# Kernel tuning notes

Hardware: AMD Instinct MI355X
Metric: run time of the kernel (lower is better)

## Reference

```python
import jax, jax.numpy as jnp
import numpy as np

BN_EPS = 1e-3      # Keras BatchNormalization default epsilon
LRELU_ALPHA = 0.3  # Keras LeakyReLU default alpha


def _bn(x, gamma, beta, mean, var):
    # inference-mode batch norm over the feature (last) axis
    return gamma * (x - mean) * jax.lax.rsqrt(var + BN_EPS) + beta


def _gcn(x, adj, w, b):
    # spektral GCNConv: A_hat @ (X @ W) + b   (adj assumed pre-normalized)
    xw = jnp.einsum('bnf,fc->bnc', x, w)
    return jnp.einsum('bnm,bmc->bnc', adj, xw) + b


def _lrelu(x):
    return jnp.where(x >= 0, x, LRELU_ALPHA * x)


def setup_inputs() -> dict:
    key = jax.random.key(0)
    ks = jax.random.split(key, 12)
    B, N, C = 16, 1024, 256
    x = jax.random.normal(ks[0], (B, N, C), dtype=jnp.float32)
    # roughly row-normalized dense adjacency (stands in for D^-1/2 (A+I) D^-1/2)
    adj = jax.random.uniform(ks[1], (B, N, N), dtype=jnp.float32) / N
    s = 1.0 / np.sqrt(C)
    return {
        'x': x,
        'adj': adj,
        'bn1_gamma': jnp.ones((C,), jnp.float32),
        'bn1_beta': jnp.zeros((C,), jnp.float32),
        'bn1_mean': jax.random.normal(ks[2], (C,), jnp.float32) * 0.1,
        'bn1_var': jax.random.uniform(ks[3], (C,), jnp.float32) + 0.5,
        'w1': jax.random.normal(ks[4], (C, C), jnp.float32) * s,
        'b1': jnp.zeros((C,), jnp.float32),
        'bn2_gamma': jnp.ones((C,), jnp.float32),
        'bn2_beta': jnp.zeros((C,), jnp.float32),
        'bn2_mean': jax.random.normal(ks[5], (C,), jnp.float32) * 0.1,
        'bn2_var': jax.random.uniform(ks[6], (C,), jnp.float32) + 0.5,
        'w2': jax.random.normal(ks[7], (C, C), jnp.float32) * s,
        'b2': jnp.zeros((C,), jnp.float32),
        'w_skip': jax.random.normal(ks[8], (C, C), jnp.float32) * s,
        'b_skip': jnp.zeros((C,), jnp.float32),
    }


def reference(x, adj, bn1_gamma, bn1_beta, bn1_mean, bn1_var, w1, b1,
              bn2_gamma, bn2_beta, bn2_mean, bn2_var, w2, b2, w_skip, b_skip):
    h = _bn(x, bn1_gamma, bn1_beta, bn1_mean, bn1_var)          # BN(input)
    out = _lrelu(_gcn(h, adj, w1, b1))                          # GCNConv + LeakyReLU
    out = _bn(out, bn2_gamma, bn2_beta, bn2_mean, bn2_var)      # BN
    out = _lrelu(_gcn(out, adj, w2, b2))                        # GCNConv + LeakyReLU
    skip = _gcn(h, adj, w_skip, b_skip)                         # skip GCNConv on BN(input)
    # Dropout is identity at inference
    return out + skip
```

## Files before the change

### kernel.cpp

```cpp
#include <hip/hip_runtime.h>

#define LRELU_ALPHA 0.3f
#define BN_EPS 1e-3f

using u16 = unsigned short;
using u32 = unsigned int;

typedef __attribute__((ext_vector_type(8))) short bf16x8;
typedef __attribute__((ext_vector_type(4))) float f32x4;

struct alignas(8) U16x4 { u16 x, y, z, w; };

__device__ __forceinline__ u16 f2bf(float f) {
  union { float f; u32 u; } v; v.f = f;
  u32 b = v.u;
  b += 0x7FFFu + ((b >> 16) & 1u);
  return (u16)(b >> 16);
}
__device__ __forceinline__ float bf2f(u16 h) {
  union { u32 u; float f; } v; v.u = ((u32)h) << 16;
  return v.f;
}

typedef const __attribute__((address_space(1))) void* gas_ptr;
typedef __attribute__((address_space(3))) void* las_ptr;

__device__ __forceinline__ void gload16(const void* g, void* l) {
  __builtin_amdgcn_global_load_lds((gas_ptr)g, (las_ptr)l, 16, 0, 0);
}

template <int K>
__device__ __forceinline__ void gemm_core(const u16* __restrict__ A,
                                          const u16* __restrict__ B,
                                          u16* lds, f32x4 (&acc)[4][4]) {
  const int t = threadIdx.x, lane = t & 63, wid = t >> 6;
  const int wm = (wid >> 1) * 64, wn = (wid & 1) * 64;
  const int lrow = lane & 15, lk = (lane >> 4) * 8;
  const int r0 = t >> 3, ce = (t & 7) * 8, lo = wid * 512;
  u16* ldsA = lds;
  u16* ldsB = lds + 8192;
#pragma unroll 1
  for (int kt = 0; kt < K / 64; ++kt) {
    const u16* gA = A + kt * 64;
    const u16* gB = B + kt * 64;
#pragma unroll
    for (int cc = 0; cc < 4; ++cc) {
      gload16(gA + (size_t)(cc * 32 + r0) * K + ce, ldsA + cc * 2048 + lo);
      gload16(gB + (size_t)(cc * 32 + r0) * K + ce, ldsB + cc * 2048 + lo);
    }
    asm volatile("s_waitcnt vmcnt(0)" ::: "memory");
    __syncthreads();
#pragma unroll
    for (int kk = 0; kk < 2; ++kk) {
      bf16x8 a[4], b[4];
#pragma unroll
      for (int i = 0; i < 4; ++i)
        a[i] = *(const bf16x8*)(ldsA + (wm + i * 16 + lrow) * 64 + kk * 32 + lk);
#pragma unroll
      for (int i = 0; i < 4; ++i)
        b[i] = *(const bf16x8*)(ldsB + (wn + i * 16 + lrow) * 64 + kk * 32 + lk);
#pragma unroll
      for (int i = 0; i < 4; ++i)
#pragma unroll
        for (int j = 0; j < 4; ++j)
          acc[i][j] = __builtin_amdgcn_mfma_f32_16x16x32_bf16(a[i], b[j], acc[i][j], 0, 0, 0);
    }
    __syncthreads();
  }
}

template <int K>
__device__ __forceinline__ void gemm_core64(const u16* __restrict__ A,
                                            const u16* __restrict__ B,
                                            u16* lds, f32x4 (&acc)[2][4]) {
  const int t = threadIdx.x, lane = t & 63, wid = t >> 6;
  const int wm = wid * 32;
  const int lrow = lane & 15, lk = (lane >> 4) * 8;
  const int r0 = t >> 3, ce = (t & 7) * 8, lo = wid * 512;
  u16* ldsA = lds;
  u16* ldsB = lds + 8192;
#pragma unroll 1
  for (int kt = 0; kt < K / 64; ++kt) {
    const u16* gA = A + kt * 64;
    const u16* gB = B + kt * 64;
#pragma unroll
    for (int cc = 0; cc < 4; ++cc)
      gload16(gA + (size_t)(cc * 32 + r0) * K + ce, ldsA + cc * 2048 + lo);
#pragma unroll
    for (int cc = 0; cc < 2; ++cc)
      gload16(gB + (size_t)(cc * 32 + r0) * K + ce, ldsB + cc * 2048 + lo);
    asm volatile("s_waitcnt vmcnt(0)" ::: "memory");
    __syncthreads();
#pragma unroll
    for (int kk = 0; kk < 2; ++kk) {
      bf16x8 a[2], b[4];
#pragma unroll
      for (int i = 0; i < 2; ++i)
        a[i] = *(const bf16x8*)(ldsA + (wm + i * 16 + lrow) * 64 + kk * 32 + lk);
#pragma unroll
      for (int j = 0; j < 4; ++j)
        b[j] = *(const bf16x8*)(ldsB + (j * 16 + lrow) * 64 + kk * 32 + lk);
#pragma unroll
      for (int i = 0; i < 2; ++i)
#pragma unroll
        for (int j = 0; j < 4; ++j)
          acc[i][j] = __builtin_amdgcn_mfma_f32_16x16x32_bf16(a[i], b[j], acc[i][j], 0, 0, 0);
    }
    __syncthreads();
  }
}

#define ACC_INIT(R)                                 \
  f32x4 acc[R][4];                                  \
  _Pragma("unroll") for (int i_ = 0; i_ < R; ++i_)  \
  _Pragma("unroll") for (int j_ = 0; j_ < 4; ++j_)  \
      acc[i_][j_] = {0.f, 0.f, 0.f, 0.f};

__global__ __launch_bounds__(256) void k_prep_h(
    const float* __restrict__ w1, const float* __restrict__ wsk, const float* __restrict__ w2,
    const float* __restrict__ g1, const float* __restrict__ be1,
    const float* __restrict__ m1, const float* __restrict__ v1,
    const float* __restrict__ g2, const float* __restrict__ be2,
    const float* __restrict__ m2, const float* __restrict__ v2,
    const float* __restrict__ x,
    u16* __restrict__ wcatT, u16* __restrict__ w2T,
    float* __restrict__ s2, float* __restrict__ t2c, u16* __restrict__ h_bf) {
  int bid = blockIdx.x;
  if (bid < 768) {
    if (bid == 0) {
      int c = threadIdx.x;
      float a2 = g2[c] * rsqrtf(v2[c] + BN_EPS);
      s2[c] = a2;
      t2c[c] = be2[c] - m2[c] * a2;
    }
    int i = bid * 256 + threadIdx.x;
    if (i < 131072) {
      int co = i >> 8, ci = i & 255;
      const float* w = (co < 256) ? w1 : wsk;
      wcatT[i] = f2bf(w[ci * 256 + (co & 255)]);
    } else {
      int k = i - 131072;
      int co = k >> 8, ci = k & 255;
      w2T[k] = f2bf(w2[ci * 256 + co]);
    }
  } else {
    int base = (bid - 768) * 256 + threadIdx.x;
    int c0 = (base << 2) & 255;
    float sc[4], sh[4];
#pragma unroll
    for (int u = 0; u < 4; ++u) {
      int c = c0 + u;
      float a = g1[c] * rsqrtf(v1[c] + BN_EPS);
      sc[u] = a;
      sh[u] = be1[c] - m1[c] * a;
    }
#pragma unroll
    for (int j = 0; j < 16; ++j) {
      int k = j * 65536 + base;
      float4 v = ((const float4*)x)[k];
      U16x4 o = {f2bf(v.x * sc[0] + sh[0]), f2bf(v.y * sc[1] + sh[1]),
                 f2bf(v.z * sc[2] + sh[2]), f2bf(v.w * sc[3] + sh[3])};
      ((U16x4*)h_bf)[k] = o;
    }
  }
}

__global__ __launch_bounds__(256) void k_xw_cvt(const float* __restrict__ adj,
                                                u16* __restrict__ adj_bf,
                                                const u16* __restrict__ h_bf,
                                                const u16* __restrict__ wcatT,
                                                u16* __restrict__ hwT) {
  __shared__ u16 lds[17408];
  const int bid = blockIdx.x;
  const int r = bid % 5;
  if (r == 4) {
    const int stripe = bid / 5;
    const float4* src = (const float4*)adj + (size_t)stripe * 32768;
    U16x4* dst = (U16x4*)adj_bf + (size_t)stripe * 32768;
    for (int i = threadIdx.x; i < 32768; i += 256) {
      float4 v = src[i];
      U16x4 o = {f2bf(v.x), f2bf(v.y), f2bf(v.z), f2bf(v.w)};
      dst[i] = o;
    }
    return;
  }
  const int mt = bid / 5, nt = r;
  ACC_INIT(4);
  gemm_core<256>(h_bf + (size_t)mt * 128 * 256, wcatT + (size_t)nt * 128 * 256, lds, acc);

  const int t = threadIdx.x, lane = t & 63, wid = t >> 6;
  const int row0 = (wid >> 1) * 64 + (lane >> 4) * 4;
  const int col0 = (wid & 1) * 64 + (lane & 15);
  __syncthreads();
  u16* tl = lds;
#pragma unroll
  for (int j = 0; j < 4; ++j) {
    int co_l = col0 + j * 16;
#pragma unroll
    for (int i = 0; i < 4; ++i)
#pragma unroll
      for (int q = 0; q < 4; ++q)
        tl[co_l * 136 + row0 + i * 16 + q] = f2bf(acc[i][j][q]);
  }
  __syncthreads();
  const int rw = t >> 4, seg = t & 15;
  const int b = mt >> 3, nb = (mt & 7) * 128;
#pragma unroll
  for (int p = 0; p < 8; ++p) {
    int co_l = p * 16 + rw;
    *(bf16x8*)(hwT + (((size_t)(b * 512 + nt * 128 + co_l)) << 10) + nb + seg * 8) =
        *(const bf16x8*)(tl + co_l * 136 + seg * 8);
  }
}

__global__ __launch_bounds__(256) void k_big1(const u16* __restrict__ adj_bf,
                                              const u16* __restrict__ hwT,
                                              const float* __restrict__ b1,
                                              const float* __restrict__ bsk,
                                              const float* __restrict__ s2,
                                              const float* __restrict__ t2c,
                                              u16* __restrict__ u2b,
                                              u16* __restrict__ skipb) {
  __shared__ u16 lds[17408];
  ACC_INIT(4);
  const int mt = blockIdx.x, nt = blockIdx.y, bz = blockIdx.z;
  gemm_core<1024>(adj_bf + ((size_t)bz << 20) + (size_t)mt * 128 * 1024,
                  hwT    + ((size_t)bz << 19) + (size_t)nt * 128 * 1024, lds, acc);

  const int t = threadIdx.x, lane = t & 63, wid = t >> 6;
  const int row0 = (wid >> 1) * 64 + (lane >> 4) * 4;
  const int col0 = (wid & 1) * 64 + (lane & 15);
  const bool conv = (nt < 2);
  const int cb = (nt & 1) * 128;
  __syncthreads();
  u16* tl = lds;
#pragma unroll
  for (int j = 0; j < 4; ++j) {
    int cl = col0 + j * 16;
    int c = cb + cl;
    float bias = conv ? b1[c] : bsk[c];
    float sc = s2[c], tc = t2c[c];
#pragma unroll
    for (int i = 0; i < 4; ++i)
#pragma unroll
      for (int q = 0; q < 4; ++q) {
        float y = acc[i][j][q] + bias;
        float v;
        if (conv) {
          float u = (y >= 0.f) ? y : LRELU_ALPHA * y;
          v = fmaf(u, sc, tc);
        } else {
          v = y;
        }
        tl[(row0 + i * 16 + q) * 136 + cl] = f2bf(v);
      }
  }
  __syncthreads();
  u16* dstbase = (conv ? u2b : skipb) + ((size_t)bz << 18) + cb;
  const int rw = t >> 4, seg = t & 15;
  const int nb = mt * 128;
#pragma unroll
  for (int p = 0; p < 8; ++p) {
    int nl = p * 16 + rw;
    *(bf16x8*)(dstbase + ((size_t)(nb + nl) << 8) + seg * 8) =
        *(const bf16x8*)(tl + nl * 136 + seg * 8);
  }
}

__global__ __launch_bounds__(256) void k_sm2(const u16* __restrict__ w2T,
                                             const u16* __restrict__ u2b,
                                             u16* __restrict__ t2T) {
  __shared__ u16 lds[12288];
  ACC_INIT(2);
  const int mt = blockIdx.x, nt = blockIdx.y, bz = blockIdx.z;
  gemm_core64<256>(w2T + (size_t)mt * 128 * 256,
                   u2b + ((size_t)bz << 18) + (size_t)nt * 64 * 256, lds, acc);

  const int t = threadIdx.x, lane = t & 63, wid = t >> 6;
  const int row0 = wid * 32 + (lane >> 4) * 4;
  const int col0 = lane & 15;
  __syncthreads();
  u16* tl = lds;
#pragma unroll
  for (int j = 0; j < 4; ++j)
#pragma unroll
    for (int i = 0; i < 2; ++i)
#pragma unroll
      for (int q = 0; q < 4; ++q)
        tl[(row0 + i * 16 + q) * 72 + col0 + j * 16] = f2bf(acc[i][j][q]);
  __syncthreads();
  u16* base = t2T + ((size_t)bz << 18) + nt * 64;
  const int rw = t >> 3, seg = t & 7;
#pragma unroll
  for (int p = 0; p < 4; ++p) {
    int co = p * 32 + rw;
    *(bf16x8*)(base + (((size_t)(mt * 128 + co)) << 10) + seg * 8) =
        *(const bf16x8*)(tl + co * 72 + seg * 8);
  }
}

__global__ __launch_bounds__(256) void k_big2(const u16* __restrict__ adj_bf,
                                              const u16* __restrict__ t2T,
                                              const float* __restrict__ b2,
                                              const u16* __restrict__ skipb,
                                              float* __restrict__ outp) {
  __shared__ u16 lds[17408];
  ACC_INIT(2);
  const int mt = blockIdx.x, nt = blockIdx.y, bz = blockIdx.z;
  gemm_core64<1024>(adj_bf + ((size_t)bz << 20) + (size_t)mt * 128 * 1024,
                    t2T    + ((size_t)bz << 18) + (size_t)nt * 64 * 1024, lds, acc);

  const int t = threadIdx.x, lane = t & 63, wid = t >> 6;
  const int row0 = wid * 32 + (lane >> 4) * 4;
  const int col0 = lane & 15;
  __syncthreads();
  float* tf = (float*)lds;
#pragma unroll
  for (int j = 0; j < 4; ++j) {
    int cl = col0 + j * 16;
    float bias = b2[nt * 64 + cl];
#pragma unroll
    for (int i = 0; i < 2; ++i)
#pragma unroll
      for (int q = 0; q < 4; ++q) {
        float y = acc[i][j][q] + bias;
        tf[(row0 + i * 16 + q) * 68 + cl] = (y >= 0.f) ? y : LRELU_ALPHA * y;
      }
  }
  __syncthreads();
  const int rw = t >> 4, seg = t & 15;
#pragma unroll
  for (int p = 0; p < 8; ++p) {
    int nl = p * 16 + rw;
    size_t go = ((size_t)bz << 18) + ((size_t)(mt * 128 + nl) << 8) + nt * 64 + seg * 4;
    float4 v = *(const float4*)(tf + nl * 68 + seg * 4);
    U16x4 sk = *(const U16x4*)(skipb + go);
    float4 o = {v.x + bf2f(sk.x), v.y + bf2f(sk.y), v.z + bf2f(sk.z), v.w + bf2f(sk.w)};
    *(float4*)(outp + go) = o;
  }
}

extern "C" void kernel_launch(void* const* d_in, const int* in_sizes, int n_in,
                              void* d_out, int out_size, void* d_ws, size_t ws_size,
                              hipStream_t stream) {
  const float* x   = (const float*)d_in[0];
  const float* adj = (const float*)d_in[1];
  const float* g1  = (const float*)d_in[2];
  const float* be1 = (const float*)d_in[3];
  const float* mu1 = (const float*)d_in[4];
  const float* v1  = (const float*)d_in[5];
  const float* w1  = (const float*)d_in[6];
  const float* b1  = (const float*)d_in[7];
  const float* g2  = (const float*)d_in[8];
  const float* be2 = (const float*)d_in[9];
  const float* mu2 = (const float*)d_in[10];
  const float* v2  = (const float*)d_in[11];
  const float* w2  = (const float*)d_in[12];
  const float* b2  = (const float*)d_in[13];
  const float* wsk = (const float*)d_in[14];
  const float* bsk = (const float*)d_in[15];
  float* out = (float*)d_out;

  char* ws = (char*)d_ws;
  u16*   adj_bf = (u16*)(ws);
  u16*   hwT    = (u16*)(ws + 33554432);
  u16*   h_bf   = (u16*)(ws + 50331648);
  u16*   u2b    = (u16*)(ws + 58720256);
  u16*   t2T    = (u16*)(ws + 67108864);
  u16*   skipb  = (u16*)(ws + 75497472);
  u16*   wcatT  = (u16*)(ws + 83886080);
  u16*   w2T    = (u16*)(ws + 84148224);
  float* s2     = (float*)(ws + 84281344);
  float* t2c    = (float*)(ws + 84282368);
  if (ws_size < 84283392) return;

  k_prep_h <<<1024, 256, 0, stream>>>(w1, wsk, w2, g1, be1, mu1, v1, g2, be2, mu2, v2,
                                      x, wcatT, w2T, s2, t2c, h_bf);
  k_xw_cvt <<<640, 256, 0, stream>>>(adj, adj_bf, h_bf, wcatT, hwT);
  k_big1<<<dim3(8, 4, 16),  256, 0, stream>>>(adj_bf, hwT, b1, bsk, s2, t2c, u2b, skipb);
  k_sm2 <<<dim3(2, 16, 16), 256, 0, stream>>>(w2T, u2b, t2T);
  k_big2<<<dim3(8, 4, 16),  256, 0, stream>>>(adj_bf, t2T, b2, skipb, out);
}
```

Baseline: 242.2 us.

## Split adjacency conversion from XW GEMM and add XCD-aware block swizzle

The fused kernel that interleaved fp32-to-bf16 adjacency conversion blocks with XW GEMM tiles is split into a grid-stride conversion kernel and a separate GEMM kernel. The three GEMM kernels now use a 1D grid with a remap so that consecutive blocks dispatched to the same XCD share the same batch, which aims to improve L2 reuse of the adjacency and the right-hand operand. The split adds one kernel launch and removes the overlap between the bandwidth-bound conversion and the compute-bound GEMM.

```diff
diff --git a/kernel.cpp b/kernel.cpp
--- a/kernel.cpp
+++ b/kernel.cpp
@@ -27,6 +27,10 @@
 
 __device__ __forceinline__ void gload16(const void* g, void* l) {
   __builtin_amdgcn_global_load_lds((gas_ptr)g, (las_ptr)l, 16, 0, 0);
+}
+
+__device__ __forceinline__ int xcd_swz512(int lid) {
+  return (lid & 7) * 64 + (lid >> 3);
 }
 
 template <int K>
@@ -165,26 +169,23 @@
   }
 }
 
-__global__ __launch_bounds__(256) void k_xw_cvt(const float* __restrict__ adj,
-                                                u16* __restrict__ adj_bf,
-                                                const u16* __restrict__ h_bf,
-                                                const u16* __restrict__ wcatT,
-                                                u16* __restrict__ hwT) {
+__global__ __launch_bounds__(256) void k_cvt(const float* __restrict__ adj,
+                                             u16* __restrict__ adj_bf) {
+  const int N4 = 4194304;
+  int stride = gridDim.x * blockDim.x;
+  for (int idx = blockIdx.x * blockDim.x + threadIdx.x; idx < N4; idx += stride) {
+    float4 v = ((const float4*)adj)[idx];
+    U16x4 o = {f2bf(v.x), f2bf(v.y), f2bf(v.z), f2bf(v.w)};
+    ((U16x4*)adj_bf)[idx] = o;
+  }
+}
+
+__global__ __launch_bounds__(256) void k_xw(const u16* __restrict__ h_bf,
+                                            const u16* __restrict__ wcatT,
+                                            u16* __restrict__ hwT) {
   __shared__ u16 lds[17408];
-  const int bid = blockIdx.x;
-  const int r = bid % 5;
-  if (r == 4) {
-    const int stripe = bid / 5;
-    const float4* src = (const float4*)adj + (size_t)stripe * 32768;
-    U16x4* dst = (U16x4*)adj_bf + (size_t)stripe * 32768;
-    for (int i = threadIdx.x; i < 32768; i += 256) {
-      float4 v = src[i];
-      U16x4 o = {f2bf(v.x), f2bf(v.y), f2bf(v.z), f2bf(v.w)};
-      dst[i] = o;
-    }
-    return;
-  }
-  const int mt = bid / 5, nt = r;
+  const int wg = xcd_swz512(blockIdx.x);
+  const int mt = wg >> 2, nt = wg & 3;
   ACC_INIT(4);
   gemm_core<256>(h_bf + (size_t)mt * 128 * 256, wcatT + (size_t)nt * 128 * 256, lds, acc);
 
@@ -223,7 +224,8 @@
                                               u16* __restrict__ skipb) {
   __shared__ u16 lds[17408];
   ACC_INIT(4);
-  const int mt = blockIdx.x, nt = blockIdx.y, bz = blockIdx.z;
+  const int wg = xcd_swz512(blockIdx.x);
+  const int mt = wg & 7, nt = (wg >> 3) & 3, bz = wg >> 5;
   gemm_core<1024>(adj_bf + ((size_t)bz << 20) + (size_t)mt * 128 * 1024,
                   hwT    + ((size_t)bz << 19) + (size_t)nt * 128 * 1024, lds, acc);
 
@@ -306,7 +308,8 @@
                                               float* __restrict__ outp) {
   __shared__ u16 lds[17408];
   ACC_INIT(2);
-  const int mt = blockIdx.x, nt = blockIdx.y, bz = blockIdx.z;
+  const int wg = xcd_swz512(blockIdx.x);
+  const int mt = wg & 7, nt = (wg >> 3) & 3, bz = wg >> 5;
   gemm_core64<1024>(adj_bf + ((size_t)bz << 20) + (size_t)mt * 128 * 1024,
                     t2T    + ((size_t)bz << 18) + (size_t)nt * 64 * 1024, lds, acc);
 
@@ -376,8 +379,9 @@
 
   k_prep_h <<<1024, 256, 0, stream>>>(w1, wsk, w2, g1, be1, mu1, v1, g2, be2, mu2, v2,
                                       x, wcatT, w2T, s2, t2c, h_bf);
-  k_xw_cvt <<<640, 256, 0, stream>>>(adj, adj_bf, h_bf, wcatT, hwT);
-  k_big1<<<dim3(8, 4, 16),  256, 0, stream>>>(adj_bf, hwT, b1, bsk, s2, t2c, u2b, skipb);
+  k_cvt    <<<2048, 256, 0, stream>>>(adj, adj_bf);
+  k_xw     <<<512,  256, 0, stream>>>(h_bf, wcatT, hwT);
+  k_big1   <<<512,  256, 0, stream>>>(adj_bf, hwT, b1, bsk, s2, t2c, u2b, skipb);
   k_sm2 <<<dim3(2, 16, 16), 256, 0, stream>>>(w2T, u2b, t2T);
-  k_big2<<<dim3(8, 4, 16),  256, 0, stream>>>(adj_bf, t2T, b2, skipb, out);
-}
+  k_big2   <<<512,  256, 0, stream>>>(adj_bf, t2T, b2, skipb, out);
+}
```

Result: faster. 210.7 us (-13.0%).
